# Optimization experiments

Measured on AMD Instinct MI355X. Metric: run time of the kernel, lower is better.

## Reference

```python
import jax, jax.numpy as jnp
import numpy as np

B, D_IN, UNITS, KFEAT = 2048, 2048, 1024, 49


def setup_inputs() -> dict:
    key = jax.random.key(0)
    ks = jax.random.split(key, 10)
    s = 0.02  # small init scale to keep sigmoids/tanh unsaturated
    return {
        "inputs": jax.random.normal(ks[0], (B, D_IN), jnp.float32),
        "h_tm": jax.random.normal(ks[1], (B, UNITS), jnp.float32),
        "m_tm": jax.random.normal(ks[2], (B, UNITS), jnp.float32),
        "v_seq": jax.random.normal(ks[3], (B, KFEAT, UNITS), jnp.float32),
        # gate weights stacked along output dim in order [f, i, o, g, a]
        "W_gates": jax.random.normal(ks[4], (UNITS, 5 * UNITS), jnp.float32) * s,
        "U_gates": jax.random.normal(ks[5], (D_IN, 5 * UNITS), jnp.float32) * s,
        "b_gates": jnp.zeros((5 * UNITS,), jnp.float32),
        "W_z": jax.random.normal(ks[6], (UNITS, KFEAT + 1), jnp.float32) * s,
        "U_z": jax.random.normal(ks[7], (UNITS, KFEAT + 1), jnp.float32) * s,
        "W_h": jax.random.normal(ks[8], (KFEAT + 1, 1), jnp.float32) * s,
    }


def reference(inputs, h_tm, m_tm, v_seq, W_gates, U_gates, b_gates, W_z, U_z, W_h):
    U = h_tm.shape[-1]
    # fused gate pre-activations: [B, 5U]
    z = h_tm @ W_gates + inputs @ U_gates + b_gates
    f, i, o, g, a = (z[:, j * U:(j + 1) * U] for j in range(5))
    ft = jax.nn.sigmoid(f)
    it = jax.nn.sigmoid(i)
    ot = jax.nn.sigmoid(o)
    gt = jax.nn.sigmoid(g)
    at = jnp.tanh(a)
    mt = m_tm * ft + it * at               # memory cell
    tanh_mt = jnp.tanh(mt)
    ht = ot * tanh_mt                      # hidden state
    st = gt * tanh_mt                      # visual sentinel
    # sentinel-augmented features: [B, K+1, U]
    v_expand = jnp.concatenate([v_seq, st[:, None, :]], axis=1)
    vtt = jnp.einsum('bku,uz->bkz', v_expand, W_z)   # [B, K+1, K+1]
    dtt = (ht @ U_z)[:, None, :]                     # broadcast over K+1 (K.repeat)
    zt = jnp.einsum('bkz,zo->bko', jnp.tanh(vtt + dtt), W_h)  # [B, K+1, 1]
    # NOTE: original uses keras softmax with default axis=-1 on a size-1 axis
    alpha_t = jax.nn.softmax(zt, axis=-1)            # [B, K+1, 1]
    ct = jnp.sum(alpha_t * v_expand, axis=1)         # batch_dot(axes=1) + squeeze
    return (ht + ct, ht, mt)
```

## Files before the change

kernel.cpp:

```cpp
#include <hip/hip_runtime.h>
#include <stdint.h>

#define BB   2048
#define DIN  2048
#define UU   1024
#define KF   49
#define GM   2048
#define GK   3072
#define GN   5120

typedef __bf16  bf16x8 __attribute__((ext_vector_type(8)));
typedef float   f32x4  __attribute__((ext_vector_type(4)));

static __device__ __forceinline__ unsigned short f2bf(float f) {
    union { float f; unsigned u; } x; x.f = f;
    unsigned u = x.u;
    unsigned r = (u + 0x7fffu + ((u >> 16) & 1u)) >> 16;
    return (unsigned short)r;
}

__global__ void prep(const float* __restrict__ h, const float* __restrict__ x,
                     const float* __restrict__ Wg, const float* __restrict__ Ug,
                     unsigned short* __restrict__ A, unsigned short* __restrict__ Wt) {
    __shared__ float t[32][36];
    if (blockIdx.x < 6144) {
        int idx = blockIdx.x * 256 + threadIdx.x;
        int b = idx / (GK / 4);
        int k = (idx % (GK / 4)) * 4;
        float4 v;
        if (k < UU) v = *(const float4*)(h + (size_t)b * UU + k);
        else        v = *(const float4*)(x + (size_t)b * DIN + (k - UU));
        ushort4 o;
        o.x = f2bf(v.x); o.y = f2bf(v.y); o.z = f2bf(v.z); o.w = f2bf(v.w);
        *(ushort4*)(A + (size_t)idx * 4) = o;
    } else {
        int bid2 = blockIdx.x - 6144;
        int k0 = (bid2 % (GK / 32)) * 32;
        int n0 = (bid2 / (GK / 32)) * 32;
        int r  = threadIdx.x >> 3;
        int cq = threadIdx.x & 7;
        int k = k0 + r;
        const float* src = (k < UU) ? (Wg + (size_t)k * GN) : (Ug + (size_t)(k - UU) * GN);
        *(float4*)&t[r][cq * 4] = *(const float4*)(src + n0 + cq * 4);
        __syncthreads();
        ushort4 o;
        o.x = f2bf(t[cq * 4 + 0][r]);
        o.y = f2bf(t[cq * 4 + 1][r]);
        o.z = f2bf(t[cq * 4 + 2][r]);
        o.w = f2bf(t[cq * 4 + 3][r]);
        *(ushort4*)(Wt + (size_t)(n0 + r) * GK + k0 + cq * 4) = o;
    }
}

__global__ void vsum_kernel(const float* __restrict__ v_seq, float* __restrict__ vsum) {
    const int b = blockIdx.x;
    const int u = threadIdx.x * 4;
    const float* vp = v_seq + (size_t)b * KF * UU + u;
    float4 a = *(const float4*)(vp);
#pragma unroll 8
    for (int k = 1; k < KF; k++) {
        float4 v = *(const float4*)(vp + (size_t)k * UU);
        a.x += v.x; a.y += v.y; a.z += v.z; a.w += v.w;
    }
    *(float4*)(vsum + (size_t)b * UU + u) = a;
}

__global__ __launch_bounds__(256, 2) void gemm_fused(
        const unsigned short* __restrict__ A, const unsigned short* __restrict__ Wt,
        const float* __restrict__ m_tm, const float* __restrict__ bg,
        const float* __restrict__ vsum, float* __restrict__ out) {
    __shared__ __align__(16) char lds[18432];

    const int tid  = threadIdx.x;
    const int lane = tid & 63;
    const int wave = tid >> 6;
    const int wr = wave >> 1, wc = wave & 1;
    const int brow  = blockIdx.y * 128;
    const int ucol0 = blockIdx.x * 32;

    f32x4 acc[4][5];
#pragma unroll
    for (int m = 0; m < 4; m++)
#pragma unroll
        for (int g = 0; g < 5; g++) acc[m][g] = (f32x4){0.f, 0.f, 0.f, 0.f};

    const unsigned short* src[5];
    int ldsoff[5];
    bool valid[5];
#pragma unroll
    for (int t = 0; t < 5; t++) {
        int base = t * 256 + wave * 64;
        int j = base + lane;
        valid[t]  = (base < 1152);
        ldsoff[t] = j * 16;
        if (j < 512) {
            src[t] = A + (size_t)(brow + (j >> 2)) * GK + (j & 3) * 8;
        } else {
            int j2 = j - 512;
            int g = j2 >> 7;
            int n = (j2 >> 2) & 31;
            int c = j2 & 3;
            int gg = (g > 4) ? 4 : g;
            src[t] = Wt + ((size_t)gg * UU + ucol0 + n) * GK + c * 8;
        }
    }

    for (int k0 = 0; k0 < GK; k0 += 32) {
#pragma unroll
        for (int t = 0; t < 5; t++)
            if (valid[t])
                __builtin_amdgcn_global_load_lds(
                    (const __attribute__((address_space(1))) void*)(src[t] + k0),
                    (__attribute__((address_space(3))) void*)(lds + ldsoff[t]), 16, 0, 0);
        __syncthreads();

        bf16x8 af[4], bfg[5];
#pragma unroll
        for (int m = 0; m < 4; m++)
            af[m] = *(const bf16x8*)(lds + (wr * 64 + m * 16 + (lane & 15)) * 64 + (lane >> 4) * 16);
#pragma unroll
        for (int g = 0; g < 5; g++)
            bfg[g] = *(const bf16x8*)(lds + 8192 + g * 2048 + (wc * 16 + (lane & 15)) * 64 + (lane >> 4) * 16);
#pragma unroll
        for (int m = 0; m < 4; m++)
#pragma unroll
            for (int g = 0; g < 5; g++)
                acc[m][g] = __builtin_amdgcn_mfma_f32_16x16x32_bf16(af[m], bfg[g], acc[m][g], 0, 0, 0);
        __syncthreads();
    }

    const int ucol = ucol0 + wc * 16 + (lane & 15);
    const float b0 = bg[0 * UU + ucol];
    const float b1 = bg[1 * UU + ucol];
    const float b2 = bg[2 * UU + ucol];
    const float b3 = bg[3 * UU + ucol];
    const float b4 = bg[4 * UU + ucol];
    const int r0 = brow + wr * 64 + ((lane >> 4) << 2);
    float* out0 = out;
    float* out1 = out + (size_t)GM * UU;
    float* out2 = out + 2 * (size_t)GM * UU;
#pragma unroll
    for (int m = 0; m < 4; m++) {
#pragma unroll
        for (int j = 0; j < 4; j++) {
            const int row = r0 + m * 16 + j;
            const size_t idx = (size_t)row * UU + ucol;
            const float mtm = m_tm[idx];
            const float vs  = vsum[idx];
            const float f = acc[m][0][j] + b0;
            const float i = acc[m][1][j] + b1;
            const float o = acc[m][2][j] + b2;
            const float g = acc[m][3][j] + b3;
            const float a = acc[m][4][j] + b4;
            const float ft = 1.f / (1.f + __expf(-f));
            const float it = 1.f / (1.f + __expf(-i));
            const float ot = 1.f / (1.f + __expf(-o));
            const float gt = 1.f / (1.f + __expf(-g));
            const float at = tanhf(a);
            const float mtv = mtm * ft + it * at;
            const float tm  = tanhf(mtv);
            const float ht  = ot * tm;
            const float st  = gt * tm;
            out0[idx] = ht + vs + st;
            out1[idx] = ht;
            out2[idx] = mtv;
        }
    }
}

extern "C" void kernel_launch(void* const* d_in, const int* in_sizes, int n_in,
                              void* d_out, int out_size, void* d_ws, size_t ws_size,
                              hipStream_t stream) {
    (void)in_sizes; (void)n_in; (void)out_size; (void)ws_size;
    const float* inputs  = (const float*)d_in[0];
    const float* h_tm    = (const float*)d_in[1];
    const float* m_tm    = (const float*)d_in[2];
    const float* v_seq   = (const float*)d_in[3];
    const float* W_gates = (const float*)d_in[4];
    const float* U_gates = (const float*)d_in[5];
    const float* b_gates = (const float*)d_in[6];

    char* ws = (char*)d_ws;
    unsigned short* Abf = (unsigned short*)ws;
    unsigned short* Wt  = (unsigned short*)(ws + 12582912);
    float*          vs  = (float*)(ws + 12582912 + 31457280);
    float* out = (float*)d_out;

    hipLaunchKernelGGL(prep, dim3(6144 + (GK / 32) * (GN / 32)), dim3(256), 0, stream,
                       h_tm, inputs, W_gates, U_gates, Abf, Wt);
    hipLaunchKernelGGL(vsum_kernel, dim3(BB), dim3(256), 0, stream, v_seq, vs);
    hipLaunchKernelGGL(gemm_fused, dim3(UU / 32, GM / 128), dim3(256), 0, stream,
                       Abf, Wt, m_tm, b_gates, vs, out);
}
```

Before: 223.3 us.

## Fuse v_seq feature summation into the gated GEMM main loop

Removes the separate vsum kernel and its workspace round-trip. Each GEMM block now accumulates the sum of v_seq over the feature axis for its 128x32 output tile, spread across the K-loop iterations. The partial sums are staged in the reused LDS buffer and read in the epilogue. This overlaps the large v_seq stream with MFMA work and drops one launch plus the intermediate write and read. In exchange it adds strided 128-byte global loads and register pressure inside the GEMM loop.

```diff
diff --git a/kernel.cpp b/kernel.cpp
--- a/kernel.cpp
+++ b/kernel.cpp
@@ -52,23 +52,10 @@
     }
 }
 
-__global__ void vsum_kernel(const float* __restrict__ v_seq, float* __restrict__ vsum) {
-    const int b = blockIdx.x;
-    const int u = threadIdx.x * 4;
-    const float* vp = v_seq + (size_t)b * KF * UU + u;
-    float4 a = *(const float4*)(vp);
-#pragma unroll 8
-    for (int k = 1; k < KF; k++) {
-        float4 v = *(const float4*)(vp + (size_t)k * UU);
-        a.x += v.x; a.y += v.y; a.z += v.z; a.w += v.w;
-    }
-    *(float4*)(vsum + (size_t)b * UU + u) = a;
-}
-
 __global__ __launch_bounds__(256, 2) void gemm_fused(
         const unsigned short* __restrict__ A, const unsigned short* __restrict__ Wt,
         const float* __restrict__ m_tm, const float* __restrict__ bg,
-        const float* __restrict__ vsum, float* __restrict__ out) {
+        const float* __restrict__ v_seq, float* __restrict__ out) {
     __shared__ __align__(16) char lds[18432];
 
     const int tid  = threadIdx.x;
@@ -105,6 +92,11 @@
         }
     }
 
+    float4 vacc[4];
+#pragma unroll
+    for (int r = 0; r < 4; r++) vacc[r] = (float4){0.f, 0.f, 0.f, 0.f};
+    const float* vp = v_seq + ((size_t)(brow + (tid >> 3)) * KF) * UU + ucol0 + (tid & 7) * 4;
+
     for (int k0 = 0; k0 < GK; k0 += 32) {
 #pragma unroll
         for (int t = 0; t < 5; t++)
@@ -112,6 +104,22 @@
                 __builtin_amdgcn_global_load_lds(
                     (const __attribute__((address_space(1))) void*)(src[t] + k0),
                     (__attribute__((address_space(3))) void*)(lds + ldsoff[t]), 16, 0, 0);
+
+        {
+            const int kk = k0 >> 6;
+            const float4 va0 = *(const float4*)(vp + ((size_t)0  * KF + kk) * UU);
+            const float4 va1 = *(const float4*)(vp + ((size_t)32 * KF + kk) * UU);
+            const float4 vb0 = *(const float4*)(vp + ((size_t)64 * KF + kk) * UU);
+            const float4 vb1 = *(const float4*)(vp + ((size_t)96 * KF + kk) * UU);
+            if (((k0 >> 5) & 1) == 0) {
+                vacc[0].x += va0.x; vacc[0].y += va0.y; vacc[0].z += va0.z; vacc[0].w += va0.w;
+                vacc[1].x += va1.x; vacc[1].y += va1.y; vacc[1].z += va1.z; vacc[1].w += va1.w;
+            } else {
+                vacc[2].x += vb0.x; vacc[2].y += vb0.y; vacc[2].z += vb0.z; vacc[2].w += vb0.w;
+                vacc[3].x += vb1.x; vacc[3].y += vb1.y; vacc[3].z += vb1.z; vacc[3].w += vb1.w;
+            }
+        }
+
         __syncthreads();
 
         bf16x8 af[4], bfg[5];
@@ -129,13 +137,30 @@
         __syncthreads();
     }
 
+#pragma unroll
+    for (int r = 0; r < 4; r++) {
+        const float4 v = *(const float4*)(vp + ((size_t)(32 * r) * KF + 48) * UU);
+        vacc[r].x += v.x; vacc[r].y += v.y; vacc[r].z += v.z; vacc[r].w += v.w;
+    }
+
+    float* lv = (float*)lds;
+    {
+        const int lr = tid >> 3, lc = (tid & 7) * 4;
+#pragma unroll
+        for (int r = 0; r < 4; r++)
+            *(float4*)&lv[(size_t)(lr + 32 * r) * 36 + lc] = vacc[r];
+    }
+    __syncthreads();
+
     const int ucol = ucol0 + wc * 16 + (lane & 15);
+    const int lcol = wc * 16 + (lane & 15);
     const float b0 = bg[0 * UU + ucol];
     const float b1 = bg[1 * UU + ucol];
     const float b2 = bg[2 * UU + ucol];
     const float b3 = bg[3 * UU + ucol];
     const float b4 = bg[4 * UU + ucol];
     const int r0 = brow + wr * 64 + ((lane >> 4) << 2);
+    const int lr0 = wr * 64 + ((lane >> 4) << 2);
     float* out0 = out;
     float* out1 = out + (size_t)GM * UU;
     float* out2 = out + 2 * (size_t)GM * UU;
@@ -145,8 +170,8 @@
         for (int j = 0; j < 4; j++) {
             const int row = r0 + m * 16 + j;
             const size_t idx = (size_t)row * UU + ucol;
+            const float vs  = lv[(size_t)(lr0 + m * 16 + j) * 36 + lcol];
             const float mtm = m_tm[idx];
-            const float vs  = vsum[idx];
             const float f = acc[m][0][j] + b0;
             const float i = acc[m][1][j] + b1;
             const float o = acc[m][2][j] + b2;
@@ -183,12 +208,10 @@
     char* ws = (char*)d_ws;
     unsigned short* Abf = (unsigned short*)ws;
     unsigned short* Wt  = (unsigned short*)(ws + 12582912);
-    float*          vs  = (float*)(ws + 12582912 + 31457280);
     float* out = (float*)d_out;
 
     hipLaunchKernelGGL(prep, dim3(6144 + (GK / 32) * (GN / 32)), dim3(256), 0, stream,
                        h_tm, inputs, W_gates, U_gates, Abf, Wt);
-    hipLaunchKernelGGL(vsum_kernel, dim3(BB), dim3(256), 0, stream, v_seq, vs);
     hipLaunchKernelGGL(gemm_fused, dim3(UU / 32, GM / 128), dim3(256), 0, stream,
-                       Abf, Wt, m_tm, b_gates, vs, out);
-}
+                       Abf, Wt, m_tm, b_gates, v_seq, out);
+}
```

Measured after the change: 209.3 us. 6.3% less time.

## Fuse v_seq reduction into GEMM via producer waves and triple-buffer the K loop

Applied to the files above, without the earlier changes.

Drops the separate vsum kernel. Four extra waves per block now stream v_seq and reduce it over K while the four GEMM waves compute, and the sums pass to the epilogue through LDS. The GEMM loop changes from single-buffered with two barriers per step to a three-stage LDS ring with explicit vmcnt waits. The weight layout is interleaved per unit so each block's five gate columns are contiguous. The block doubles to 512 threads and LDS grows, which may lower occupancy, and the hand-written waitcnt scheduling is fragile.

```diff
diff --git a/kernel.cpp b/kernel.cpp
--- a/kernel.cpp
+++ b/kernel.cpp
@@ -9,8 +9,18 @@
 #define GK   3072
 #define GN   5120
 
+#define BM   128
+#define UC   32
+#define BKS  32
+#define SZB  18432
+#define LVOFF (3 * SZB)
+
 typedef __bf16  bf16x8 __attribute__((ext_vector_type(8)));
 typedef float   f32x4  __attribute__((ext_vector_type(4)));
+
+#define VL(dst, ptr) asm volatile("global_load_dwordx4 %0, %1, off" \
+                                  : "=v"(dst) : "v"(ptr) : "memory")
+#define WAITVM(n) asm volatile("s_waitcnt vmcnt(" #n ")" ::: "memory")
 
 static __device__ __forceinline__ unsigned short f2bf(float f) {
     union { float f; unsigned u; } x; x.f = f;
@@ -43,41 +53,33 @@
         const float* src = (k < UU) ? (Wg + (size_t)k * GN) : (Ug + (size_t)(k - UU) * GN);
         *(float4*)&t[r][cq * 4] = *(const float4*)(src + n0 + cq * 4);
         __syncthreads();
+        int n = n0 + r;
+        int u = n & (UU - 1);
+        int g = n >> 10;
         ushort4 o;
         o.x = f2bf(t[cq * 4 + 0][r]);
         o.y = f2bf(t[cq * 4 + 1][r]);
         o.z = f2bf(t[cq * 4 + 2][r]);
         o.w = f2bf(t[cq * 4 + 3][r]);
-        *(ushort4*)(Wt + (size_t)(n0 + r) * GK + k0 + cq * 4) = o;
-    }
-}
-
-__global__ void vsum_kernel(const float* __restrict__ v_seq, float* __restrict__ vsum) {
-    const int b = blockIdx.x;
-    const int u = threadIdx.x * 4;
-    const float* vp = v_seq + (size_t)b * KF * UU + u;
-    float4 a = *(const float4*)(vp);
-#pragma unroll 8
-    for (int k = 1; k < KF; k++) {
-        float4 v = *(const float4*)(vp + (size_t)k * UU);
-        a.x += v.x; a.y += v.y; a.z += v.z; a.w += v.w;
-    }
-    *(float4*)(vsum + (size_t)b * UU + u) = a;
-}
-
-__global__ __launch_bounds__(256, 2) void gemm_fused(
+        *(ushort4*)(Wt + (size_t)(u * 5 + g) * GK + k0 + cq * 4) = o;
+    }
+}
+
+__global__ __launch_bounds__(512, 2) void gemm_fused(
         const unsigned short* __restrict__ A, const unsigned short* __restrict__ Wt,
         const float* __restrict__ m_tm, const float* __restrict__ bg,
-        const float* __restrict__ vsum, float* __restrict__ out) {
-    __shared__ __align__(16) char lds[18432];
+        const float* __restrict__ v_seq, float* __restrict__ out) {
+    __shared__ __align__(16) char lds[3 * SZB + 18432];
 
     const int tid  = threadIdx.x;
     const int lane = tid & 63;
     const int wave = tid >> 6;
-    const int wr = wave >> 1, wc = wave & 1;
-    const int brow  = blockIdx.y * 128;
-    const int ucol0 = blockIdx.x * 32;
-
+    const bool isg = (wave < 4);
+    const int brow  = blockIdx.y * BM;
+    const int ucol0 = blockIdx.x * UC;
+
+    const int wr = (wave >> 1) & 1;
+    const int wc = wave & 1;
     f32x4 acc[4][5];
 #pragma unroll
     for (int m = 0; m < 4; m++)
@@ -86,56 +88,112 @@
 
     const unsigned short* src[5];
     int ldsoff[5];
-    bool valid[5];
-#pragma unroll
-    for (int t = 0; t < 5; t++) {
-        int base = t * 256 + wave * 64;
-        int j = base + lane;
-        valid[t]  = (base < 1152);
-        ldsoff[t] = j * 16;
-        if (j < 512) {
-            src[t] = A + (size_t)(brow + (j >> 2)) * GK + (j & 3) * 8;
-        } else {
-            int j2 = j - 512;
-            int g = j2 >> 7;
-            int n = (j2 >> 2) & 31;
-            int c = j2 & 3;
-            int gg = (g > 4) ? 4 : g;
-            src[t] = Wt + ((size_t)gg * UU + ucol0 + n) * GK + c * 8;
+    {
+        const int gt = tid & 255;
+#pragma unroll
+        for (int r = 0; r < 5; ++r) {
+            if (r < 2) {
+                int j = r * 256 + gt;
+                src[r] = A + (size_t)(brow + (j >> 2)) * GK + (j & 3) * 8;
+                ldsoff[r] = j * 16;
+            } else {
+                int j2 = (r < 4) ? (r - 2) * 256 + gt : 512 + (gt & 127);
+                src[r] = Wt + (size_t)((size_t)ucol0 * 5 + (j2 >> 2)) * GK + (j2 & 3) * 8;
+                ldsoff[r] = 8192 + j2 * 16;
+            }
         }
     }
-
-    for (int k0 = 0; k0 < GK; k0 += 32) {
-#pragma unroll
-        for (int t = 0; t < 5; t++)
-            if (valid[t])
-                __builtin_amdgcn_global_load_lds(
-                    (const __attribute__((address_space(1))) void*)(src[t] + k0),
-                    (__attribute__((address_space(3))) void*)(lds + ldsoff[t]), 16, 0, 0);
-        __syncthreads();
-
-        bf16x8 af[4], bfg[5];
+    const int aoff = (wr * 64 + (lane & 15)) * 64 + (lane >> 4) * 16;
+    const int boff = 8192 + ((wc * 16 + (lane & 15)) * 5) * 64 + (lane >> 4) * 16;
+
+    auto STAGE5 = [&](int ko, int bufb) {
+#pragma unroll
+        for (int r = 0; r < 5; ++r)
+            __builtin_amdgcn_global_load_lds(
+                (const __attribute__((address_space(1))) void*)(src[r] + ko),
+                (__attribute__((address_space(3))) void*)(lds + bufb + ldsoff[r]), 16, 0, 0);
+    };
+    auto COMPUTE = [&](int bufb) {
+        bf16x8 af[4], bfr[5];
+#pragma unroll
+        for (int m = 0; m < 4; m++) af[m]  = *(const bf16x8*)(lds + bufb + aoff + m * 1024);
+#pragma unroll
+        for (int g = 0; g < 5; g++) bfr[g] = *(const bf16x8*)(lds + bufb + boff + g * 64);
 #pragma unroll
         for (int m = 0; m < 4; m++)
-            af[m] = *(const bf16x8*)(lds + (wr * 64 + m * 16 + (lane & 15)) * 64 + (lane >> 4) * 16);
-#pragma unroll
-        for (int g = 0; g < 5; g++)
-            bfg[g] = *(const bf16x8*)(lds + 8192 + g * 2048 + (wc * 16 + (lane & 15)) * 64 + (lane >> 4) * 16);
-#pragma unroll
-        for (int m = 0; m < 4; m++)
 #pragma unroll
             for (int g = 0; g < 5; g++)
-                acc[m][g] = __builtin_amdgcn_mfma_f32_16x16x32_bf16(af[m], bfg[g], acc[m][g], 0, 0, 0);
-        __syncthreads();
-    }
-
+                acc[m][g] = __builtin_amdgcn_mfma_f32_16x16x32_bf16(af[m], bfr[g], acc[m][g], 0, 0, 0);
+    };
+
+    const int stid = tid & 255;
+    const float* vp = v_seq + (size_t)(brow + (stid >> 1)) * (KF * UU)
+                    + ucol0 + (stid & 1) * 16;
+    f32x4 qa0, qa1, qa2, qa3, qb0, qb1, qb2, qb3;
+    f32x4 s0 = {0,0,0,0}, s1 = {0,0,0,0}, s2 = {0,0,0,0}, s3 = {0,0,0,0};
+
+#define VQUAD(q0_,q1_,q2_,q3_, kk) do { const float* p_ = vp + (size_t)(kk) * UU; \
+    VL(q0_, p_); VL(q1_, p_ + 4); VL(q2_, p_ + 8); VL(q3_, p_ + 12); } while (0)
+#define SCONS(q0_,q1_,q2_,q3_) do { s0 += q0_; s1 += q1_; s2 += q2_; s3 += q3_; } while (0)
+#define BAR() do { __builtin_amdgcn_s_barrier(); __builtin_amdgcn_sched_barrier(0); } while (0)
+
+    if (isg) { STAGE5(0, 0); STAGE5(BKS, SZB); WAITVM(5); }
+    else     { VQUAD(qa0, qa1, qa2, qa3, 0); }
+    BAR();
+
+    int cb = 0, sb = 2 * SZB, ko = 2 * BKS;
+#define ADV() do { cb += SZB; if (cb == 3 * SZB) cb = 0; \
+                   sb += SZB; if (sb == 3 * SZB) sb = 0; ko += BKS; } while (0)
+
+    for (int grp = 0; grp < 23; ++grp) {
+        if (isg) { STAGE5(ko, sb); COMPUTE(cb); WAITVM(5); }
+        else { VQUAD(qb0, qb1, qb2, qb3, 2 * grp + 1); WAITVM(4);
+               __builtin_amdgcn_sched_barrier(0); SCONS(qa0, qa1, qa2, qa3); }
+        BAR(); ADV();
+        if (isg) { STAGE5(ko, sb); COMPUTE(cb); WAITVM(5); }
+        BAR(); ADV();
+        if (isg) { STAGE5(ko, sb); COMPUTE(cb); WAITVM(5); }
+        else { VQUAD(qa0, qa1, qa2, qa3, 2 * grp + 2); WAITVM(4);
+               __builtin_amdgcn_sched_barrier(0); SCONS(qb0, qb1, qb2, qb3); }
+        BAR(); ADV();
+        if (isg) { STAGE5(ko, sb); COMPUTE(cb); WAITVM(5); }
+        BAR(); ADV();
+    }
+    if (isg) { STAGE5(ko, sb); COMPUTE(cb); WAITVM(5); }
+    else { VQUAD(qb0, qb1, qb2, qb3, 47); WAITVM(4);
+           __builtin_amdgcn_sched_barrier(0); SCONS(qa0, qa1, qa2, qa3); }
+    BAR(); ADV();
+    if (isg) { STAGE5(ko, sb); COMPUTE(cb); WAITVM(5); }
+    BAR(); ADV();
+    if (isg) { COMPUTE(cb); WAITVM(0); }
+    else { VQUAD(qa0, qa1, qa2, qa3, 48); WAITVM(4);
+           __builtin_amdgcn_sched_barrier(0); SCONS(qb0, qb1, qb2, qb3); }
+    BAR(); ADV();
+    if (isg) { COMPUTE(cb); }
+    else {
+        WAITVM(0);
+        __builtin_amdgcn_sched_barrier(0);
+        SCONS(qa0, qa1, qa2, qa3);
+        float* lvp = (float*)(lds + LVOFF);
+        const int row = stid >> 1, cbase = (stid & 1) * 16;
+        *(f32x4*)&lvp[row * 36 + cbase +  0] = s0;
+        *(f32x4*)&lvp[row * 36 + cbase +  4] = s1;
+        *(f32x4*)&lvp[row * 36 + cbase +  8] = s2;
+        *(f32x4*)&lvp[row * 36 + cbase + 12] = s3;
+        asm volatile("s_waitcnt lgkmcnt(0)" ::: "memory");
+    }
+    __builtin_amdgcn_s_barrier();
+    if (!isg) return;
+
+    const float* lvp = (const float*)(lds + LVOFF);
     const int ucol = ucol0 + wc * 16 + (lane & 15);
-    const float b0 = bg[0 * UU + ucol];
-    const float b1 = bg[1 * UU + ucol];
-    const float b2 = bg[2 * UU + ucol];
-    const float b3 = bg[3 * UU + ucol];
-    const float b4 = bg[4 * UU + ucol];
-    const int r0 = brow + wr * 64 + ((lane >> 4) << 2);
+    const int lcol = wc * 16 + (lane & 15);
+    const float c0 = bg[0 * UU + ucol];
+    const float c1 = bg[1 * UU + ucol];
+    const float c2 = bg[2 * UU + ucol];
+    const float c3 = bg[3 * UU + ucol];
+    const float c4 = bg[4 * UU + ucol];
+    const int lr0 = wr * 64 + ((lane >> 4) << 2);
     float* out0 = out;
     float* out1 = out + (size_t)GM * UU;
     float* out2 = out + 2 * (size_t)GM * UU;
@@ -143,15 +201,16 @@
     for (int m = 0; m < 4; m++) {
 #pragma unroll
         for (int j = 0; j < 4; j++) {
-            const int row = r0 + m * 16 + j;
+            const int lrow = lr0 + m * 16 + j;
+            const int row  = brow + lrow;
             const size_t idx = (size_t)row * UU + ucol;
+            const float vs  = lvp[lrow * 36 + lcol];
             const float mtm = m_tm[idx];
-            const float vs  = vsum[idx];
-            const float f = acc[m][0][j] + b0;
-            const float i = acc[m][1][j] + b1;
-            const float o = acc[m][2][j] + b2;
-            const float g = acc[m][3][j] + b3;
-            const float a = acc[m][4][j] + b4;
+            const float f = acc[m][0][j] + c0;
+            const float i = acc[m][1][j] + c1;
+            const float o = acc[m][2][j] + c2;
+            const float g = acc[m][3][j] + c3;
+            const float a = acc[m][4][j] + c4;
             const float ft = 1.f / (1.f + __expf(-f));
             const float it = 1.f / (1.f + __expf(-i));
             const float ot = 1.f / (1.f + __expf(-o));
@@ -183,12 +242,10 @@
     char* ws = (char*)d_ws;
     unsigned short* Abf = (unsigned short*)ws;
     unsigned short* Wt  = (unsigned short*)(ws + 12582912);
-    float*          vs  = (float*)(ws + 12582912 + 31457280);
     float* out = (float*)d_out;
 
     hipLaunchKernelGGL(prep, dim3(6144 + (GK / 32) * (GN / 32)), dim3(256), 0, stream,
                        h_tm, inputs, W_gates, U_gates, Abf, Wt);
-    hipLaunchKernelGGL(vsum_kernel, dim3(BB), dim3(256), 0, stream, v_seq, vs);
-    hipLaunchKernelGGL(gemm_fused, dim3(UU / 32, GM / 128), dim3(256), 0, stream,
-                       Abf, Wt, m_tm, b_gates, vs, out);
-}
+    hipLaunchKernelGGL(gemm_fused, dim3(UU / UC, GM / BM), dim3(512), 0, stream,
+                       Abf, Wt, m_tm, b_gates, v_seq, out);
+}
```

Result: no change. 220.0 us (-1.5%).

## Co-schedule v_seq reduction with double-buffered swizzled GEMM in one launch

Applied to the files above, without the earlier changes.

Merges the v_seq sum over the feature axis into the GEMM launch, interleaving streaming blocks with GEMM blocks so the memory-bound reduction overlaps the MFMA-bound GEMM. The GEMM tile shrinks to 64 rows, its LDS is double-buffered so the next k-step's global loads are issued before the current step's compute, and an XOR swizzle is applied to the LDS layout to reduce bank conflicts. Because GEMM blocks can no longer read vsum, a separate fixup kernel adds vsum into the first output afterwards. This costs an extra read-modify-write pass over the output and an extra launch, and the smaller tile raises operand traffic per FLOP.

```diff
diff --git a/kernel.cpp b/kernel.cpp
--- a/kernel.cpp
+++ b/kernel.cpp
@@ -9,8 +9,16 @@
 #define GK   3072
 #define GN   5120
 
+#define BKS  32
+#define SZB  14336
+
+#define NGEMM 1024
+#define NSTRM 2048
+
 typedef __bf16  bf16x8 __attribute__((ext_vector_type(8)));
 typedef float   f32x4  __attribute__((ext_vector_type(4)));
+
+#define WAITVM0() asm volatile("s_waitcnt vmcnt(0)" ::: "memory")
 
 static __device__ __forceinline__ unsigned short f2bf(float f) {
     union { float f; unsigned u; } x; x.f = f;
@@ -52,106 +60,133 @@
     }
 }
 
-__global__ void vsum_kernel(const float* __restrict__ v_seq, float* __restrict__ vsum) {
-    const int b = blockIdx.x;
-    const int u = threadIdx.x * 4;
-    const float* vp = v_seq + (size_t)b * KF * UU + u;
-    float4 a = *(const float4*)(vp);
-#pragma unroll 8
-    for (int k = 1; k < KF; k++) {
-        float4 v = *(const float4*)(vp + (size_t)k * UU);
-        a.x += v.x; a.y += v.y; a.z += v.z; a.w += v.w;
-    }
-    *(float4*)(vsum + (size_t)b * UU + u) = a;
-}
-
-__global__ __launch_bounds__(256, 2) void gemm_fused(
+__global__ __launch_bounds__(256, 3) void kernel2(
         const unsigned short* __restrict__ A, const unsigned short* __restrict__ Wt,
         const float* __restrict__ m_tm, const float* __restrict__ bg,
-        const float* __restrict__ vsum, float* __restrict__ out) {
-    __shared__ __align__(16) char lds[18432];
-
-    const int tid  = threadIdx.x;
+        const float* __restrict__ v_seq, float* __restrict__ vsum,
+        float* __restrict__ out) {
+    __shared__ __align__(16) char lds[2 * SZB];
+
+    const int tid = threadIdx.x;
+    const int bid = blockIdx.x;
+    const int sel = bid % 3;
+
+    if (sel != 0) {
+        const int row = (bid / 3) * 2 + (sel - 1);
+        const float* vp = v_seq + (size_t)row * (KF * UU) + tid * 4;
+        f32x4 s = *(const f32x4*)(vp);
+#pragma unroll 8
+        for (int k = 1; k < KF; ++k)
+            s += *(const f32x4*)(vp + (size_t)k * UU);
+        *(f32x4*)(vsum + (size_t)row * UU + tid * 4) = s;
+        return;
+    }
+
+    const int gb   = bid / 3;
     const int lane = tid & 63;
     const int wave = tid >> 6;
     const int wr = wave >> 1, wc = wave & 1;
-    const int brow  = blockIdx.y * 128;
-    const int ucol0 = blockIdx.x * 32;
-
-    f32x4 acc[4][5];
-#pragma unroll
-    for (int m = 0; m < 4; m++)
+    const int brow  = (gb >> 5) * 64;
+    const int ucol0 = (gb & 31) * 32;
+
+    f32x4 acc[2][5];
+#pragma unroll
+    for (int m = 0; m < 2; m++)
 #pragma unroll
         for (int g = 0; g < 5; g++) acc[m][g] = (f32x4){0.f, 0.f, 0.f, 0.f};
 
-    const unsigned short* src[5];
-    int ldsoff[5];
-    bool valid[5];
-#pragma unroll
-    for (int t = 0; t < 5; t++) {
-        int base = t * 256 + wave * 64;
-        int j = base + lane;
-        valid[t]  = (base < 1152);
-        ldsoff[t] = j * 16;
-        if (j < 512) {
-            src[t] = A + (size_t)(brow + (j >> 2)) * GK + (j & 3) * 8;
+    const unsigned short* src[4];
+    int ldsoff[4];
+#pragma unroll
+    for (int r = 0; r < 4; ++r) {
+        if (r == 0) {
+            int j = tid;
+            int row = j >> 2;
+            int kq = (j & 3) ^ ((row >> 1) & 3);
+            src[r] = A + (size_t)(brow + row) * GK + kq * 8;
+            ldsoff[r] = j * 16;
         } else {
-            int j2 = j - 512;
-            int g = j2 >> 7;
-            int n = (j2 >> 2) & 31;
-            int c = j2 & 3;
-            int gg = (g > 4) ? 4 : g;
-            src[t] = Wt + ((size_t)gg * UU + ucol0 + n) * GK + c * 8;
+            int j2 = (r < 3) ? (r - 1) * 256 + tid : 512 + (tid & 127);
+            int rB = j2 >> 2;
+            int kq = (j2 & 3) ^ ((rB >> 1) & 3);
+            int g = rB >> 5, n = rB & 31;
+            src[r] = Wt + ((size_t)g * UU + ucol0 + n) * GK + kq * 8;
+            ldsoff[r] = 4096 + j2 * 16;
         }
     }
 
-    for (int k0 = 0; k0 < GK; k0 += 32) {
-#pragma unroll
-        for (int t = 0; t < 5; t++)
-            if (valid[t])
-                __builtin_amdgcn_global_load_lds(
-                    (const __attribute__((address_space(1))) void*)(src[t] + k0),
-                    (__attribute__((address_space(3))) void*)(lds + ldsoff[t]), 16, 0, 0);
-        __syncthreads();
-
-        bf16x8 af[4], bfg[5];
-#pragma unroll
-        for (int m = 0; m < 4; m++)
-            af[m] = *(const bf16x8*)(lds + (wr * 64 + m * 16 + (lane & 15)) * 64 + (lane >> 4) * 16);
-#pragma unroll
-        for (int g = 0; g < 5; g++)
-            bfg[g] = *(const bf16x8*)(lds + 8192 + g * 2048 + (wc * 16 + (lane & 15)) * 64 + (lane >> 4) * 16);
-#pragma unroll
-        for (int m = 0; m < 4; m++)
+    int aoff[2], boff[5];
+#pragma unroll
+    for (int m = 0; m < 2; m++) {
+        int row = wr * 32 + m * 16 + (lane & 15);
+        aoff[m] = row * 64 + (((lane >> 4) ^ ((row >> 1) & 3)) * 16);
+    }
+#pragma unroll
+    for (int g = 0; g < 5; g++) {
+        int rB = g * 32 + wc * 16 + (lane & 15);
+        boff[g] = 4096 + rB * 64 + (((lane >> 4) ^ ((rB >> 1) & 3)) * 16);
+    }
+
+    auto STAGE = [&](int kstep, int bufb) {
+        const int ko = kstep * BKS;
+#pragma unroll
+        for (int r = 0; r < 4; ++r)
+            __builtin_amdgcn_global_load_lds(
+                (const __attribute__((address_space(1))) void*)(src[r] + ko),
+                (__attribute__((address_space(3))) void*)(lds + bufb + ldsoff[r]), 16, 0, 0);
+    };
+    auto COMPUTE = [&](int bufb) {
+        bf16x8 af[2], bfr[5];
+#pragma unroll
+        for (int m = 0; m < 2; m++) af[m]  = *(const bf16x8*)(lds + bufb + aoff[m]);
+#pragma unroll
+        for (int g = 0; g < 5; g++) bfr[g] = *(const bf16x8*)(lds + bufb + boff[g]);
+#pragma unroll
+        for (int m = 0; m < 2; m++)
 #pragma unroll
             for (int g = 0; g < 5; g++)
-                acc[m][g] = __builtin_amdgcn_mfma_f32_16x16x32_bf16(af[m], bfg[g], acc[m][g], 0, 0, 0);
-        __syncthreads();
+                acc[m][g] = __builtin_amdgcn_mfma_f32_16x16x32_bf16(af[m], bfr[g], acc[m][g], 0, 0, 0);
+    };
+
+    STAGE(0, 0);
+    WAITVM0();
+    __builtin_amdgcn_s_barrier();
+    __builtin_amdgcn_sched_barrier(0);
+
+    int buf = 0;
+    for (int t = 0; t < 96; ++t) {
+        if (t < 95) STAGE(t + 1, buf ^ SZB);
+        COMPUTE(buf);
+        if (t < 95) {
+            WAITVM0();
+            __builtin_amdgcn_s_barrier();
+            __builtin_amdgcn_sched_barrier(0);
+        }
+        buf ^= SZB;
     }
 
     const int ucol = ucol0 + wc * 16 + (lane & 15);
-    const float b0 = bg[0 * UU + ucol];
-    const float b1 = bg[1 * UU + ucol];
-    const float b2 = bg[2 * UU + ucol];
-    const float b3 = bg[3 * UU + ucol];
-    const float b4 = bg[4 * UU + ucol];
-    const int r0 = brow + wr * 64 + ((lane >> 4) << 2);
+    const float c0 = bg[0 * UU + ucol];
+    const float c1 = bg[1 * UU + ucol];
+    const float c2 = bg[2 * UU + ucol];
+    const float c3 = bg[3 * UU + ucol];
+    const float c4 = bg[4 * UU + ucol];
+    const int r0 = brow + wr * 32 + ((lane >> 4) << 2);
     float* out0 = out;
     float* out1 = out + (size_t)GM * UU;
     float* out2 = out + 2 * (size_t)GM * UU;
 #pragma unroll
-    for (int m = 0; m < 4; m++) {
+    for (int m = 0; m < 2; m++) {
 #pragma unroll
         for (int j = 0; j < 4; j++) {
             const int row = r0 + m * 16 + j;
             const size_t idx = (size_t)row * UU + ucol;
             const float mtm = m_tm[idx];
-            const float vs  = vsum[idx];
-            const float f = acc[m][0][j] + b0;
-            const float i = acc[m][1][j] + b1;
-            const float o = acc[m][2][j] + b2;
-            const float g = acc[m][3][j] + b3;
-            const float a = acc[m][4][j] + b4;
+            const float f = acc[m][0][j] + c0;
+            const float i = acc[m][1][j] + c1;
+            const float o = acc[m][2][j] + c2;
+            const float g = acc[m][3][j] + c3;
+            const float a = acc[m][4][j] + c4;
             const float ft = 1.f / (1.f + __expf(-f));
             const float it = 1.f / (1.f + __expf(-i));
             const float ot = 1.f / (1.f + __expf(-o));
@@ -161,11 +196,18 @@
             const float tm  = tanhf(mtv);
             const float ht  = ot * tm;
             const float st  = gt * tm;
-            out0[idx] = ht + vs + st;
+            out0[idx] = ht + st;
             out1[idx] = ht;
             out2[idx] = mtv;
         }
     }
+}
+
+__global__ void fixup(float* __restrict__ out0, const float* __restrict__ vsum) {
+    const size_t i = ((size_t)blockIdx.x * 256 + threadIdx.x) * 4;
+    f32x4 a = *(const f32x4*)(out0 + i);
+    a += *(const f32x4*)(vsum + i);
+    *(f32x4*)(out0 + i) = a;
 }
 
 extern "C" void kernel_launch(void* const* d_in, const int* in_sizes, int n_in,
@@ -188,7 +230,7 @@
 
     hipLaunchKernelGGL(prep, dim3(6144 + (GK / 32) * (GN / 32)), dim3(256), 0, stream,
                        h_tm, inputs, W_gates, U_gates, Abf, Wt);
-    hipLaunchKernelGGL(vsum_kernel, dim3(BB), dim3(256), 0, stream, v_seq, vs);
-    hipLaunchKernelGGL(gemm_fused, dim3(UU / 32, GM / 128), dim3(256), 0, stream,
-                       Abf, Wt, m_tm, b_gates, vs, out);
-}
+    hipLaunchKernelGGL(kernel2, dim3(NGEMM + NSTRM), dim3(256), 0, stream,
+                       Abf, Wt, m_tm, b_gates, v_seq, vs, out);
+    hipLaunchKernelGGL(fixup, dim3(BB), dim3(256), 0, stream, out, vs);
+}
```

After: 260.7 us. 1.17x slower.
